# Kernel tuning notes

Hardware: AMD Instinct MI355X
Metric: run time of the kernel (lower is better)

The kernel has to match this reference:

```python
import jax, jax.numpy as jnp
import numpy as np
from jax import lax

NPG = 61      # nodes (electrodes) per graph, hard-coded by 61*hidden reshape
B = 128       # graphs per batch
L = 160       # raw signal length -> final conv length 1
NF = 64       # num_features
HC = 128      # hidden_channels
NCLS = 4


def setup_inputs() -> dict:
    key = jax.random.key(0)
    ks = jax.random.split(key, 16)
    N = B * NPG
    # fully-connected (no self-loops) edges within each graph -> 3660 edges/graph
    a = np.repeat(np.arange(NPG), NPG)
    b = np.tile(np.arange(NPG), NPG)
    m = a != b
    sl, dl = a[m], b[m]
    off = (np.arange(B) * NPG)[:, None]
    edge_index = np.stack([(sl[None] + off).ravel(), (dl[None] + off).ravel()]).astype(np.int64)
    batch = np.repeat(np.arange(B), NPG).astype(np.int64)

    def rn(k, shape, fan_in):
        return jax.random.normal(k, shape, jnp.float32) / np.sqrt(fan_in).astype(np.float32)

    return dict(
        x=jax.random.normal(ks[0], (N, L), jnp.float32),
        edge_index=jnp.asarray(edge_index),
        batch=jnp.asarray(batch),
        edge_features=jax.random.normal(ks[1], (edge_index.shape[1], 3), jnp.float32),
        conv_w0=rn(ks[2], (NF, 1, 7), 7.0), conv_b0=jnp.zeros((NF,), jnp.float32),
        conv_w1=rn(ks[3], (NF, NF, 5), NF * 5.0), conv_b1=jnp.zeros((NF,), jnp.float32),
        conv_w2=rn(ks[4], (NF, NF, 3), NF * 3.0), conv_b2=jnp.zeros((NF,), jnp.float32),
        bn1_g=jnp.ones((NF,), jnp.float32), bn1_b=jnp.zeros((NF,), jnp.float32),
        g_w0=rn(ks[5], (NF, HC), float(NF)), g_b0=jnp.zeros((HC,), jnp.float32),
        g_w1=rn(ks[6], (HC, HC), float(HC)), g_b1=jnp.zeros((HC,), jnp.float32),
        g_w2=rn(ks[7], (HC, HC), float(HC)), g_b2=jnp.zeros((HC,), jnp.float32),
        bn2_g=jnp.ones((HC,), jnp.float32), bn2_b=jnp.zeros((HC,), jnp.float32),
        lin_w0=rn(ks[8], (NPG * HC, HC), float(NPG * HC)), lin_b0=jnp.zeros((HC,), jnp.float32),
        lin_w1=rn(ks[9], (HC, HC), float(HC)), lin_b1=jnp.zeros((HC,), jnp.float32),
        lin_w2=rn(ks[10], (HC, NCLS), float(HC)), lin_b2=jnp.zeros((NCLS,), jnp.float32),
        edge_w=rn(ks[11], (3, 1), 3.0), edge_b=jnp.zeros((1,), jnp.float32),
    )


def _conv1d(x, w, b, pad):
    # x: [N, Cin, L], w: [Cout, Cin, K]
    y = lax.conv_general_dilated(x, w, (1,), [(pad, pad)], dimension_numbers=('NCH', 'OIH', 'NCH'))
    return y + b[None, :, None]


def _maxpool7(x):
    n = x.shape[-1] // 7
    return x[..., : n * 7].reshape(x.shape[0], x.shape[1], n, 7).max(-1)


def _bn(x, g, b):
    # BatchNorm1d in training mode: biased batch statistics
    m = x.mean(0)
    v = x.var(0)
    return (x - m) * lax.rsqrt(v + 1e-5) * g + b


def _forward(x, edge_features, conv_w0, conv_b0, conv_w1, conv_b1, conv_w2, conv_b2,
             bn1_g, bn1_b, g_w0, g_b0, g_w1, g_b1, g_w2, g_b2, bn2_g, bn2_b,
             lin_w0, lin_b0, lin_w1, lin_b1, lin_w2, lin_b2, edge_w, edge_b,
             edge_index, batch):
    N = x.shape[0]
    nb = N // NPG  # == batch.max()+1 for contiguous graph layout
    # tanh-gated edge weights
    ew = jnp.tanh(edge_features @ edge_w + edge_b)            # [E, 1]
    # Conv1d feature extractor: [N,1,160] -> [N,NF,1]
    h = x[:, None, :]
    h = _maxpool7(jax.nn.relu(_conv1d(h, conv_w0, conv_b0, 0)))   # [N,NF,22]
    h = jax.nn.relu(_conv1d(h, conv_w1, conv_b1, 2))               # [N,NF,22]
    h = _maxpool7(h)                                               # [N,NF,3]
    h = _conv1d(h, conv_w2, conv_b2, 0)[:, :, 0]                   # [N,NF]
    h = _bn(h, bn1_g, bn1_b)
    # Edge-weighted GCN hops (MyzConv): lin -> gather src -> scale -> scatter-add dst
    src, dst = edge_index[0], edge_index[1]
    for w, bs, act in ((g_w0, g_b0, True), (g_w1, g_b1, True), (g_w2, g_b2, False)):
        hw = h @ w + bs                                            # [N,HC]
        msg = ew * hw[src]                                         # [E,HC]
        h = jax.ops.segment_sum(msg, dst, num_segments=N)
        if act:
            h = jax.nn.relu(h)
    h = _bn(h, bn2_g, bn2_b)
    # MLP classifier over concatenated node features per graph
    h = h.reshape(nb, NPG * HC)
    h = jax.nn.relu(h @ lin_w0 + lin_b0)
    h = jax.nn.relu(h @ lin_w1 + lin_b1)
    h = h @ lin_w2 + lin_b2
    return jax.nn.log_softmax(h, -1), ew.reshape(nb, -1).T


def reference(x, edge_index, batch, edge_features, conv_w0, conv_b0, conv_w1, conv_b1,
              conv_w2, conv_b2, bn1_g, bn1_b, g_w0, g_b0, g_w1, g_b1, g_w2, g_b2,
              bn2_g, bn2_b, lin_w0, lin_b0, lin_w1, lin_b1, lin_w2, lin_b2, edge_w, edge_b):
    return _forward(x, edge_features, conv_w0, conv_b0, conv_w1, conv_b1, conv_w2, conv_b2,
                    bn1_g, bn1_b, g_w0, g_b0, g_w1, g_b1, g_w2, g_b2, bn2_g, bn2_b,
                    lin_w0, lin_b0, lin_w1, lin_b1, lin_w2, lin_b2, edge_w, edge_b,
                    edge_index, batch)
```

## Files before the change

### kernel.cpp

```cpp
#include <hip/hip_runtime.h>
#include <math.h>

#define NPGN 61
#define NGRAPH 128
#define NNODES (NPGN*NGRAPH)
#define EPG 3660

typedef float float4v __attribute__((ext_vector_type(4)));
typedef short bf16x8 __attribute__((ext_vector_type(8)));
typedef unsigned short u16;

__device__ __forceinline__ u16 f2bf(float v){
  union { float f; unsigned u; } x; x.f = v;
  unsigned r = (x.u + 0x7FFFu + ((x.u >> 16) & 1u)) >> 16;
  return (u16)r;
}
__device__ __forceinline__ float bf2f(unsigned u){
  union { unsigned u; float f; } x; x.u = u << 16;
  return x.f;
}

__global__ __launch_bounds__(256) void k_prep(const float* __restrict__ w0,
    const float* __restrict__ w1, const float* __restrict__ w2,
    const float* __restrict__ gw0, const float* __restrict__ gw1, const float* __restrict__ gw2,
    const float* __restrict__ lw0,
    float* __restrict__ w0t, u16* __restrict__ w1b, u16* __restrict__ w2b,
    u16* __restrict__ gwt0, u16* __restrict__ gwt1, u16* __restrict__ gwt2,
    u16* __restrict__ lw0t){
  __shared__ __align__(16) u16 tile[32*132];
  int b = blockIdx.x, tid = threadIdx.x;
  if (b < 290){
    int idx = b*256 + tid;
    if (idx < 20480){
      int f = idx / 320, r = idx - f*320;
      int kk = r >> 6, c = r & 63;
      w1b[idx] = f2bf(w1[f*320 + c*5 + kk]);
    } else if (idx < 32768){
      int j = idx - 20480; w2b[j] = f2bf(w2[j]);
    } else if (idx < 40960){
      int j = idx - 32768; int jj = j >> 6, k = j & 63; gwt0[j] = f2bf(gw0[k*128 + jj]);
    } else if (idx < 57344){
      int j = idx - 40960; int jj = j >> 7, k = j & 127; gwt1[j] = f2bf(gw1[k*128 + jj]);
    } else if (idx < 73728){
      int j = idx - 57344; int jj = j >> 7, k = j & 127; gwt2[j] = f2bf(gw2[k*128 + jj]);
    } else if (idx < 74176){
      int j = idx - 73728; int k = j >> 6, f = j & 63; w0t[j] = w0[f*7 + k];
    }
  } else {
    int bb = b - 290;
    int i = bb >> 2, oq = bb & 3;
    for (int idx = tid; idx < 4096; idx += 256){
      int k = idx >> 5, ol = idx & 31;
      tile[ol*132 + k] = f2bf(lw0[((size_t)i*128 + k)*128 + oq*32 + ol]);
    }
    __syncthreads();
    unsigned* dst = (unsigned*)lw0t;
    for (int idx = tid; idx < 2048; idx += 256){
      int ol = idx >> 6, kw = idx & 63;
      unsigned v = (unsigned)tile[ol*132 + 2*kw] | ((unsigned)tile[ol*132 + 2*kw + 1] << 16);
      dst[((size_t)i*128 + oq*32 + ol)*64 + kw] = v;
    }
  }
}

#define A0T_STR 72
#define A0T_ROWS 36
#define C1_STR 24
#define NB 4
__global__ __launch_bounds__(256) void k_conv(const float* __restrict__ x,
    const float* __restrict__ w0t, const float* __restrict__ b0,
    const u16* __restrict__ w1b, const float* __restrict__ b1,
    const u16* __restrict__ w2b, const float* __restrict__ b2,
    float* __restrict__ h0, float* __restrict__ stat1p){
  int w = threadIdx.x >> 6, lane = threadIdx.x & 63;
  int tid = threadIdx.x;
  int q = lane >> 4, r16 = lane & 15;
  __shared__ __align__(16) float xs[NB][160];
  __shared__ __align__(16) u16 a0t[A0T_ROWS*A0T_STR];
  __shared__ __align__(16) u16 a1k[208];

  {
    const float* xb = x + (size_t)blockIdx.x*NB*160;
    float* xsf = &xs[0][0];
    #pragma unroll
    for (int idx = tid; idx < NB*160; idx += 256) xsf[idx] = xb[idx];
  }

  bf16x8 wf1[10], wf2[6];
  #pragma unroll
  for (int ks = 0; ks < 10; ks++)
    wf1[ks] = *(const bf16x8*)(w1b + (16*w + r16)*320 + ks*32 + q*8);
  #pragma unroll
  for (int ks = 0; ks < 6; ks++)
    wf2[ks] = *(const bf16x8*)(w2b + (16*w + r16)*192 + ks*32 + q*8);
  float4 b1v = *(const float4*)(b1 + 16*w + 4*q);
  float4 b2v = *(const float4*)(b2 + 16*w + 4*q);

  float w0r[7];
  #pragma unroll
  for (int k = 0; k < 7; k++) w0r[k] = w0t[k*64 + lane];
  float b0f = b0[lane];

  a0t[(24 + w)*A0T_STR + lane] = 0;
  __syncthreads();

  float4v sacc = {0.f,0.f,0.f,0.f}, qacc = {0.f,0.f,0.f,0.f};

  for (int i = 0; i < NB; i++){
    int n = blockIdx.x*NB + i;
    const float* xsp = &xs[i][0];

    if (w < 2) a0t[w*A0T_STR + lane] = 0;

    for (int qp = w; qp < 11; qp += 4){
      float win[20];
      #pragma unroll
      for (int j = 0; j < 20; j++) win[j] = xsp[14*qp + j];
      float m0, m1;
      #pragma unroll
      for (int r = 0; r < 7; r++){
        float s = w0r[0]*win[r];
        #pragma unroll
        for (int k = 1; k < 7; k++) s += w0r[k]*win[r+k];
        m0 = r ? fmaxf(m0, s) : s;
      }
      #pragma unroll
      for (int r = 7; r < 14; r++){
        float s = w0r[0]*win[r];
        #pragma unroll
        for (int k = 1; k < 7; k++) s += w0r[k]*win[r+k];
        m1 = (r > 7) ? fmaxf(m1, s) : s;
      }
      a0t[(2 + 2*qp)*A0T_STR + lane] = f2bf(fmaxf(m0 + b0f, 0.f));
      a0t[(3 + 2*qp)*A0T_STR + lane] = f2bf(fmaxf(m1 + b0f, 0.f));
    }
    __syncthreads();

    float4v acc0 = {0.f,0.f,0.f,0.f}, acc1 = {0.f,0.f,0.f,0.f};
    #pragma unroll
    for (int ks = 0; ks < 10; ks++){
      int kk = ks >> 1;
      int cbase = (ks & 1)*32 + q*8;
      bf16x8 bv0 = *(const bf16x8*)(a0t + (r16 + kk)*A0T_STR + cbase);
      bf16x8 bv1 = *(const bf16x8*)(a0t + (r16 + 16 + kk)*A0T_STR + cbase);
      acc0 = __builtin_amdgcn_mfma_f32_16x16x32_bf16(wf1[ks], bv0, acc0, 0, 0, 0);
      acc1 = __builtin_amdgcn_mfma_f32_16x16x32_bf16(wf1[ks], bv1, acc1, 0, 0, 0);
    }
    __syncthreads();

    u16* c1 = a0t;
    #pragma unroll
    for (int reg = 0; reg < 4; reg++){
      int m = 16*w + q*4 + reg;
      float bv_ = ((const float*)&b1v)[reg];
      c1[m*C1_STR + r16] = f2bf(fmaxf(acc0[reg] + bv_, 0.f));
      if (r16 <= 4)
        c1[m*C1_STR + 16 + r16] = f2bf(fmaxf(acc1[reg] + bv_, 0.f));
    }
    __syncthreads();

    if (w == (i & 3)){
      bf16x8 f0 = *(const bf16x8*)(c1 + lane*C1_STR);
      bf16x8 f1 = *(const bf16x8*)(c1 + lane*C1_STR + 8);
      bf16x8 f2 = *(const bf16x8*)(c1 + lane*C1_STR + 16);
      float v[24];
      #pragma unroll
      for (int j = 0; j < 8; j++){
        v[j]    = bf2f((u16)f0[j]);
        v[8+j]  = bf2f((u16)f1[j]);
        v[16+j] = bf2f((u16)f2[j]);
      }
      #pragma unroll
      for (int t = 0; t < 3; t++){
        float m = v[t*7];
        #pragma unroll
        for (int r = 1; r < 7; r++) m = fmaxf(m, v[t*7+r]);
        a1k[lane*3 + t] = f2bf(m);
      }
    }
    __syncthreads();

    float4v acc2 = {0.f,0.f,0.f,0.f};
    #pragma unroll
    for (int ks = 0; ks < 6; ks++){
      bf16x8 bs = *(const bf16x8*)(a1k + ks*32 + q*8);
      acc2 = __builtin_amdgcn_mfma_f32_16x16x32_bf16(wf2[ks], bs, acc2, 0, 0, 0);
    }
    if (r16 == 0){
      #pragma unroll
      for (int reg = 0; reg < 4; reg++){
        int f = 16*w + 4*q + reg;
        float v = acc2[reg] + ((const float*)&b2v)[reg];
        h0[(size_t)n*64 + f] = v;
        sacc[reg] += v;
        qacc[reg] += v*v;
      }
    }
  }

  if (r16 == 0){
    int bkt = blockIdx.x & 31;
    #pragma unroll
    for (int reg = 0; reg < 4; reg++){
      int f = 16*w + 4*q + reg;
      atomicAdd(&stat1p[bkt*128 + f], sacc[reg]);
      atomicAdd(&stat1p[bkt*128 + 64 + f], qacc[reg]);
    }
  }
}

#define EW_STR 72
#define HS_STR 136
#define HWT_STR 72
__global__ __launch_bounds__(512) void k_gnn(const float* __restrict__ h0,
    const float* __restrict__ stat1p,
    const float* __restrict__ bn1g, const float* __restrict__ bn1b,
    const u16* __restrict__ gwt0, const float* __restrict__ gb0,
    const u16* __restrict__ gwt1, const float* __restrict__ gb1,
    const u16* __restrict__ gwt2, const float* __restrict__ gb2,
    const float* __restrict__ ef, const float* __restrict__ eww,
    const float* __restrict__ ewb, float* __restrict__ out2,
    u16* __restrict__ hB, float* __restrict__ stat2p){
  int g = blockIdx.x, tid = threadIdx.x;
  int w = tid >> 6, lane = tid & 63, q = lane >> 4, r16 = lane & 15;
  int dt = w & 3, jh = w >> 2;
  __shared__ u16 hs[64*HS_STR];
  __shared__ u16 hwT[128*HWT_STR];
  __shared__ u16 ewl[64*EW_STR];
  __shared__ float bsc[64], bsh[64];
  __shared__ float st2[256];

  bf16x8 af0[2], af1[4], af2[4];
  #pragma unroll
  for (int ks = 0; ks < 2; ks++)
    af0[ks] = *(const bf16x8*)(gwt0 + (16*w + r16)*64 + ks*32 + q*8);
  #pragma unroll
  for (int ks = 0; ks < 4; ks++)
    af1[ks] = *(const bf16x8*)(gwt1 + (16*w + r16)*128 + ks*32 + q*8);
  #pragma unroll
  for (int ks = 0; ks < 4; ks++)
    af2[ks] = *(const bf16x8*)(gwt2 + (16*w + r16)*128 + ks*32 + q*8);
  float4 b40 = *(const float4*)(gb0 + 16*w + 4*q);
  float4 b41 = *(const float4*)(gb1 + 16*w + 4*q);
  float4 b42 = *(const float4*)(gb2 + 16*w + 4*q);

  if (tid < 64){
    float s = 0.f, s2 = 0.f;
    #pragma unroll
    for (int r = 0; r < 32; r++){
      s  += stat1p[r*128 + tid];
      s2 += stat1p[r*128 + 64 + tid];
    }
    float m = s*(1.f/NNODES), v = s2*(1.f/NNODES) - m*m;
    float sc = rsqrtf(v + 1e-5f)*bn1g[tid];
    bsc[tid] = sc; bsh[tid] = bn1b[tid] - m*sc;
  }
  if (tid < 256) st2[tid] = 0.f;
  {
    unsigned* td = (unsigned*)ewl;
    for (int idx = tid; idx < 64*EW_STR/2; idx += 512) td[idx] = 0;
  }
  {
    unsigned* hsd = (unsigned*)hs;
    for (int idx = tid; idx < 3*(HS_STR/2); idx += 512){
      int rr = 61 + idx/(HS_STR/2), cc = idx%(HS_STR/2);
      hsd[rr*(HS_STR/2) + cc] = 0;
    }
  }
  __syncthreads();

  {
    float v0 = eww[0], v1 = eww[1], v2 = eww[2], bb = ewb[0];
    const float* efg = ef + (size_t)g*EPG*3;
    for (int idx = tid; idx < EPG; idx += 512){
      const float* p = efg + idx*3;
      float v = tanhf(p[0]*v0 + p[1]*v1 + p[2]*v2 + bb);
      int s = idx/60, r = idx - s*60;
      int d = r + (r >= s ? 1 : 0);
      ewl[d*EW_STR + s] = f2bf(v);
      out2[(size_t)idx*128 + g] = v;
    }
  }
  {
    unsigned* hsd = (unsigned*)hs;
    for (int idx = tid; idx < 61*32; idx += 512){
      int i = idx >> 5, kw = idx & 31;
      float2 hv = *(const float2*)(h0 + ((size_t)g*61 + i)*64 + kw*2);
      int k0 = kw*2;
      float a = hv.x*bsc[k0] + bsh[k0];
      float b = hv.y*bsc[k0+1] + bsh[k0+1];
      hsd[i*(HS_STR/2) + kw] = (unsigned)f2bf(a) | ((unsigned)f2bf(b) << 16);
    }
  }
  __syncthreads();
  bf16x8 ewf[2];
  #pragma unroll
  for (int ks = 0; ks < 2; ks++)
    ewf[ks] = *(const bf16x8*)(ewl + (16*dt + r16)*EW_STR + ks*32 + q*8);

  #pragma unroll
  for (int nt = 0; nt < 4; nt++){
    float4v acc = {b40.x, b40.y, b40.z, b40.w};
    #pragma unroll
    for (int ks = 0; ks < 2; ks++){
      bf16x8 bv = *(const bf16x8*)(hs + (nt*16 + r16)*HS_STR + ks*32 + q*8);
      acc = __builtin_amdgcn_mfma_f32_16x16x32_bf16(af0[ks], bv, acc, 0, 0, 0);
    }
    #pragma unroll
    for (int r = 0; r < 4; r++)
      hwT[(16*w + 4*q + r)*HWT_STR + nt*16 + r16] = f2bf(acc[r]);
  }
  __syncthreads();
  #pragma unroll
  for (int nt = 0; nt < 4; nt++){
    int j = (jh*4 + nt)*16;
    float4v acc = {0.f,0.f,0.f,0.f};
    #pragma unroll
    for (int ks = 0; ks < 2; ks++){
      bf16x8 bv = *(const bf16x8*)(hwT + (j + r16)*HWT_STR + ks*32 + q*8);
      acc = __builtin_amdgcn_mfma_f32_16x16x32_bf16(ewf[ks], bv, acc, 0, 0, 0);
    }
    #pragma unroll
    for (int r = 0; r < 4; r++){
      int d = 16*dt + 4*q + r;
      hs[d*HS_STR + j + r16] = f2bf(fmaxf(acc[r], 0.f));
    }
  }
  __syncthreads();

  #pragma unroll
  for (int nt = 0; nt < 4; nt++){
    float4v acc = {b41.x, b41.y, b41.z, b41.w};
    #pragma unroll
    for (int ks = 0; ks < 4; ks++){
      bf16x8 bv = *(const bf16x8*)(hs + (nt*16 + r16)*HS_STR + ks*32 + q*8);
      acc = __builtin_amdgcn_mfma_f32_16x16x32_bf16(af1[ks], bv, acc, 0, 0, 0);
    }
    #pragma unroll
    for (int r = 0; r < 4; r++)
      hwT[(16*w + 4*q + r)*HWT_STR + nt*16 + r16] = f2bf(acc[r]);
  }
  __syncthreads();
  #pragma unroll
  for (int nt = 0; nt < 4; nt++){
    int j = (jh*4 + nt)*16;
    float4v acc = {0.f,0.f,0.f,0.f};
    #pragma unroll
    for (int ks = 0; ks < 2; ks++){
      bf16x8 bv = *(const bf16x8*)(hwT + (j + r16)*HWT_STR + ks*32 + q*8);
      acc = __builtin_amdgcn_mfma_f32_16x16x32_bf16(ewf[ks], bv, acc, 0, 0, 0);
    }
    #pragma unroll
    for (int r = 0; r < 4; r++){
      int d = 16*dt + 4*q + r;
      hs[d*HS_STR + j + r16] = f2bf(fmaxf(acc[r], 0.f));
    }
  }
  __syncthreads();

  #pragma unroll
  for (int nt = 0; nt < 4; nt++){
    float4v acc = {b42.x, b42.y, b42.z, b42.w};
    #pragma unroll
    for (int ks = 0; ks < 4; ks++){
      bf16x8 bv = *(const bf16x8*)(hs + (nt*16 + r16)*HS_STR + ks*32 + q*8);
      acc = __builtin_amdgcn_mfma_f32_16x16x32_bf16(af2[ks], bv, acc, 0, 0, 0);
    }
    #pragma unroll
    for (int r = 0; r < 4; r++)
      hwT[(16*w + 4*q + r)*HWT_STR + nt*16 + r16] = f2bf(acc[r]);
  }
  __syncthreads();
  #pragma unroll
  for (int nt = 0; nt < 4; nt++){
    int j = (jh*4 + nt)*16;
    float4v acc = {0.f,0.f,0.f,0.f};
    #pragma unroll
    for (int ks = 0; ks < 2; ks++){
      bf16x8 bv = *(const bf16x8*)(hwT + (j + r16)*HWT_STR + ks*32 + q*8);
      acc = __builtin_amdgcn_mfma_f32_16x16x32_bf16(ewf[ks], bv, acc, 0, 0, 0);
    }
    float cs = 0.f, cq = 0.f;
    #pragma unroll
    for (int r = 0; r < 4; r++){
      int d = 16*dt + 4*q + r;
      if (d < 61){
        float v = acc[r];
        hB[((size_t)g*61 + d)*128 + j + r16] = f2bf(v);
        cs += v; cq += v*v;
      }
    }
    int col = j + r16;
    atomicAdd(&st2[col], cs);
    atomicAdd(&st2[128 + col], cq);
  }
  __syncthreads();
  if (tid < 256) stat2p[(size_t)tid*128 + g] = st2[tid];
}

#define AS_STR 136
__global__ __launch_bounds__(256) void k_mlp0(const u16* __restrict__ hB,
    const float* __restrict__ stat2p,
    const float* __restrict__ bn2g, const float* __restrict__ bn2b,
    const u16* __restrict__ lw0t, float* __restrict__ y0pre){
  int bi = blockIdx.x; int i = bi >> 2, sub = bi & 3;
  int oh = sub & 1, gh = sub >> 1;
  int tid = threadIdx.x, w = tid >> 6, lane = tid & 63, q = lane >> 4, r16 = lane & 15;
  __shared__ u16 As[64*AS_STR];
  __shared__ float sc2[128], sh2[128];
  if (tid < 128){
    float4v sa = {0,0,0,0}, sb = {0,0,0,0};
    #pragma unroll
    for (int r = 0; r < 32; r++){
      sa += *(const float4v*)(stat2p + (size_t)tid*128 + r*4);
      sb += *(const float4v*)(stat2p + (size_t)(128 + tid)*128 + r*4);
    }
    float s = sa[0]+sa[1]+sa[2]+sa[3], s2 = sb[0]+sb[1]+sb[2]+sb[3];
    float m = s*(1.f/NNODES), v = s2*(1.f/NNODES) - m*m;
    float sc = rsqrtf(v + 1e-5f)*bn2g[tid];
    sc2[tid] = sc; sh2[tid] = bn2b[tid] - m*sc;
  }
  __syncthreads();
  {
    const unsigned* hbd = (const unsigned*)hB;
    unsigned* asd = (unsigned*)As;
    for (int idx = tid; idx < 4096; idx += 256){
      int gg = gh*64 + (idx >> 6), kw = idx & 63;
      unsigned pv = hbd[((size_t)gg*61 + i)*64 + kw];
      int k0 = kw*2;
      float a = bf2f(pv & 0xffffu)*sc2[k0] + sh2[k0];
      float b = bf2f(pv >> 16)*sc2[k0+1] + sh2[k0+1];
      asd[(idx >> 6)*(AS_STR/2) + kw] = (unsigned)f2bf(a) | ((unsigned)f2bf(b) << 16);
    }
  }
  __syncthreads();
  const u16* wbase = lw0t + ((size_t)i*128 + oh*64)*128;
  bf16x8 af[4];
  #pragma unroll
  for (int ks = 0; ks < 4; ks++)
    af[ks] = *(const bf16x8*)(As + (16*w + r16)*AS_STR + ks*32 + q*8);
  #pragma unroll
  for (int nt = 0; nt < 4; nt++){
    float4v acc = {0.f,0.f,0.f,0.f};
    #pragma unroll
    for (int ks = 0; ks < 4; ks++){
      bf16x8 bv = *(const bf16x8*)(wbase + (size_t)(nt*16 + r16)*128 + ks*32 + q*8);
      acc = __builtin_amdgcn_mfma_f32_16x16x32_bf16(af[ks], bv, acc, 0, 0, 0);
    }
    #pragma unroll
    for (int r = 0; r < 4; r++){
      int g = gh*64 + 16*w + 4*q + r;
      atomicAdd(&y0pre[(size_t)g*128 + oh*64 + nt*16 + r16], acc[r]);
    }
  }
}

__global__ __launch_bounds__(128) void k_mlp1(const float* __restrict__ y0pre,
    const float* __restrict__ lb0, const float* __restrict__ W1,
    const float* __restrict__ lb1, const float* __restrict__ W2,
    const float* __restrict__ lb2, float* __restrict__ out){
  int g = blockIdx.x, o = threadIdx.x;
  __shared__ float y0[128], y1[128], red[128];
  y0[o] = fmaxf(y0pre[(size_t)g*128 + o] + lb0[o], 0.f);
  __syncthreads();
  float a = lb1[o];
  #pragma unroll 8
  for (int k = 0; k < 128; k++) a += y0[k]*W1[k*128 + o];
  y1[o] = fmaxf(a, 0.f);
  __syncthreads();
  int c = o & 3, kb = o >> 2;
  float a2 = 0.f;
  #pragma unroll
  for (int j = 0; j < 4; j++){
    int k = kb + 32*j;
    a2 += y1[k]*W2[k*4 + c];
  }
  red[o] = a2;
  __syncthreads();
  #pragma unroll
  for (int off = 64; off >= 4; off >>= 1){
    if (o < off) red[o] += red[o + off];
    __syncthreads();
  }
  if (o == 0){
    float v0 = red[0]+lb2[0], v1 = red[1]+lb2[1], v2 = red[2]+lb2[2], v3 = red[3]+lb2[3];
    float m = fmaxf(fmaxf(v0,v1), fmaxf(v2,v3));
    float lse = m + logf(expf(v0-m)+expf(v1-m)+expf(v2-m)+expf(v3-m));
    out[g*4+0]=v0-lse; out[g*4+1]=v1-lse; out[g*4+2]=v2-lse; out[g*4+3]=v3-lse;
  }
}

extern "C" void kernel_launch(void* const* d_in, const int* in_sizes, int n_in,
                              void* d_out, int out_size, void* d_ws, size_t ws_size,
                              hipStream_t stream){
  const float* x    = (const float*)d_in[0];
  const float* ef   = (const float*)d_in[3];
  const float* cw0  = (const float*)d_in[4];
  const float* cb0  = (const float*)d_in[5];
  const float* cw1  = (const float*)d_in[6];
  const float* cb1  = (const float*)d_in[7];
  const float* cw2  = (const float*)d_in[8];
  const float* cb2  = (const float*)d_in[9];
  const float* bn1g = (const float*)d_in[10];
  const float* bn1b = (const float*)d_in[11];
  const float* gw0  = (const float*)d_in[12];
  const float* gb0  = (const float*)d_in[13];
  const float* gw1  = (const float*)d_in[14];
  const float* gb1  = (const float*)d_in[15];
  const float* gw2  = (const float*)d_in[16];
  const float* gb2  = (const float*)d_in[17];
  const float* bn2g = (const float*)d_in[18];
  const float* bn2b = (const float*)d_in[19];
  const float* lw0  = (const float*)d_in[20];
  const float* lb0  = (const float*)d_in[21];
  const float* lw1  = (const float*)d_in[22];
  const float* lb1  = (const float*)d_in[23];
  const float* lw2  = (const float*)d_in[24];
  const float* lb2  = (const float*)d_in[25];
  const float* eww  = (const float*)d_in[26];
  const float* ewb  = (const float*)d_in[27];
  float* out = (float*)d_out;

  float* ws   = (float*)d_ws;
  float* w1s  = ws;
  float* w2s  = w1s + 10240;
  float* w0t  = w2s + 6144;
  float* gws0 = w0t + 448;
  float* gws1 = gws0 + 4096;
  float* gws2 = gws1 + 8192;
  float* h0   = gws2 + 8192;
  float* hBs  = h0 + 499712;
  float* lw0s = hBs + 499712;
  float* accs = lw0s + 499712;

  u16* w1b    = (u16*)w1s;
  u16* w2b    = (u16*)w2s;
  u16* gwt0   = (u16*)gws0;
  u16* gwt1   = (u16*)gws1;
  u16* gwt2   = (u16*)gws2;
  u16* hB     = (u16*)hBs;
  u16* lw0t   = (u16*)lw0s;
  float* stat1p = accs;
  float* y0pre  = accs + 4096;
  float* stat2p = accs + 20480;

  hipMemsetAsync(accs, 0, 20480*sizeof(float), stream);
  k_prep <<<534, 256, 0, stream>>>(cw0, cw1, cw2, gw0, gw1, gw2, lw0,
                                   w0t, w1b, w2b, gwt0, gwt1, gwt2, lw0t);
  k_conv <<<NNODES/NB, 256, 0, stream>>>(x, w0t, cb0, w1b, cb1, w2b, cb2, h0, stat1p);
  k_gnn  <<<NGRAPH, 512, 0, stream>>>(h0, stat1p, bn1g, bn1b,
                                      gwt0, gb0, gwt1, gb1, gwt2, gb2,
                                      ef, eww, ewb, out + 512, hB, stat2p);
  k_mlp0 <<<NPGN*4, 256, 0, stream>>>(hB, stat2p, bn2g, bn2b, lw0t, y0pre);
  k_mlp1 <<<NGRAPH, 128, 0, stream>>>(y0pre, lb0, lw1, lb1, lw2, lb2, out);
}
```

Baseline: 202.2 us.

## Batch conv stages across all nodes per block to cut barriers

```diff
diff --git a/kernel.cpp b/kernel.cpp
--- a/kernel.cpp
+++ b/kernel.cpp
@@ -64,7 +64,6 @@
 }
 
 #define A0T_STR 72
-#define A0T_ROWS 36
 #define C1_STR 24
 #define NB 4
 __global__ __launch_bounds__(256) void k_conv(const float* __restrict__ x,
@@ -76,8 +75,9 @@
   int tid = threadIdx.x;
   int q = lane >> 4, r16 = lane & 15;
   __shared__ __align__(16) float xs[NB][160];
-  __shared__ __align__(16) u16 a0t[A0T_ROWS*A0T_STR];
-  __shared__ __align__(16) u16 a1k[208];
+  __shared__ __align__(16) u16 a0t[NB][36*A0T_STR];
+  __shared__ __align__(16) u16 c1s[NB][64*C1_STR];
+  __shared__ __align__(16) u16 a1k[NB][208];
 
   {
     const float* xb = x + (size_t)blockIdx.x*NB*160;
@@ -101,97 +101,100 @@
   for (int k = 0; k < 7; k++) w0r[k] = w0t[k*64 + lane];
   float b0f = b0[lane];
 
-  a0t[(24 + w)*A0T_STR + lane] = 0;
-  __syncthreads();
-
-  float4v sacc = {0.f,0.f,0.f,0.f}, qacc = {0.f,0.f,0.f,0.f};
-
-  for (int i = 0; i < NB; i++){
-    int n = blockIdx.x*NB + i;
-    const float* xsp = &xs[i][0];
-
-    if (w < 2) a0t[w*A0T_STR + lane] = 0;
-
-    for (int qp = w; qp < 11; qp += 4){
-      float win[20];
+  #pragma unroll
+  for (int i2 = 0; i2 < 6; i2++){
+    int rp = (i2 < 2) ? i2 : 22 + i2;
+    a0t[w][rp*A0T_STR + lane] = 0;
+  }
+  __syncthreads();
+
+  for (int j = w; j < 44; j += 4){
+    int n = j / 11, qp = j - n*11;
+    const float* xsp = &xs[n][0];
+    float win[20];
+    #pragma unroll
+    for (int jj = 0; jj < 20; jj++) win[jj] = xsp[14*qp + jj];
+    float m0, m1;
+    #pragma unroll
+    for (int r = 0; r < 7; r++){
+      float s = w0r[0]*win[r];
       #pragma unroll
-      for (int j = 0; j < 20; j++) win[j] = xsp[14*qp + j];
-      float m0, m1;
+      for (int k = 1; k < 7; k++) s += w0r[k]*win[r+k];
+      m0 = r ? fmaxf(m0, s) : s;
+    }
+    #pragma unroll
+    for (int r = 7; r < 14; r++){
+      float s = w0r[0]*win[r];
       #pragma unroll
-      for (int r = 0; r < 7; r++){
-        float s = w0r[0]*win[r];
-        #pragma unroll
-        for (int k = 1; k < 7; k++) s += w0r[k]*win[r+k];
-        m0 = r ? fmaxf(m0, s) : s;
-      }
-      #pragma unroll
-      for (int r = 7; r < 14; r++){
-        float s = w0r[0]*win[r];
-        #pragma unroll
-        for (int k = 1; k < 7; k++) s += w0r[k]*win[r+k];
-        m1 = (r > 7) ? fmaxf(m1, s) : s;
-      }
-      a0t[(2 + 2*qp)*A0T_STR + lane] = f2bf(fmaxf(m0 + b0f, 0.f));
-      a0t[(3 + 2*qp)*A0T_STR + lane] = f2bf(fmaxf(m1 + b0f, 0.f));
-    }
-    __syncthreads();
-
+      for (int k = 1; k < 7; k++) s += w0r[k]*win[r+k];
+      m1 = (r > 7) ? fmaxf(m1, s) : s;
+    }
+    a0t[n][(2 + 2*qp)*A0T_STR + lane] = f2bf(fmaxf(m0 + b0f, 0.f));
+    a0t[n][(3 + 2*qp)*A0T_STR + lane] = f2bf(fmaxf(m1 + b0f, 0.f));
+  }
+  __syncthreads();
+
+  #pragma unroll 1
+  for (int n = 0; n < NB; n++){
     float4v acc0 = {0.f,0.f,0.f,0.f}, acc1 = {0.f,0.f,0.f,0.f};
     #pragma unroll
     for (int ks = 0; ks < 10; ks++){
       int kk = ks >> 1;
       int cbase = (ks & 1)*32 + q*8;
-      bf16x8 bv0 = *(const bf16x8*)(a0t + (r16 + kk)*A0T_STR + cbase);
-      bf16x8 bv1 = *(const bf16x8*)(a0t + (r16 + 16 + kk)*A0T_STR + cbase);
+      bf16x8 bv0 = *(const bf16x8*)(&a0t[n][(r16 + kk)*A0T_STR + cbase]);
+      bf16x8 bv1 = *(const bf16x8*)(&a0t[n][(r16 + 16 + kk)*A0T_STR + cbase]);
       acc0 = __builtin_amdgcn_mfma_f32_16x16x32_bf16(wf1[ks], bv0, acc0, 0, 0, 0);
       acc1 = __builtin_amdgcn_mfma_f32_16x16x32_bf16(wf1[ks], bv1, acc1, 0, 0, 0);
     }
-    __syncthreads();
-
-    u16* c1 = a0t;
     #pragma unroll
     for (int reg = 0; reg < 4; reg++){
       int m = 16*w + q*4 + reg;
       float bv_ = ((const float*)&b1v)[reg];
-      c1[m*C1_STR + r16] = f2bf(fmaxf(acc0[reg] + bv_, 0.f));
+      c1s[n][m*C1_STR + r16] = f2bf(fmaxf(acc0[reg] + bv_, 0.f));
       if (r16 <= 4)
-        c1[m*C1_STR + 16 + r16] = f2bf(fmaxf(acc1[reg] + bv_, 0.f));
-    }
-    __syncthreads();
-
-    if (w == (i & 3)){
-      bf16x8 f0 = *(const bf16x8*)(c1 + lane*C1_STR);
-      bf16x8 f1 = *(const bf16x8*)(c1 + lane*C1_STR + 8);
-      bf16x8 f2 = *(const bf16x8*)(c1 + lane*C1_STR + 16);
-      float v[24];
+        c1s[n][m*C1_STR + 16 + r16] = f2bf(fmaxf(acc1[reg] + bv_, 0.f));
+    }
+  }
+  __syncthreads();
+
+  {
+    const u16* c1 = &c1s[w][0];
+    bf16x8 f0 = *(const bf16x8*)(c1 + lane*C1_STR);
+    bf16x8 f1 = *(const bf16x8*)(c1 + lane*C1_STR + 8);
+    bf16x8 f2 = *(const bf16x8*)(c1 + lane*C1_STR + 16);
+    float v[24];
+    #pragma unroll
+    for (int j = 0; j < 8; j++){
+      v[j]    = bf2f((u16)f0[j]);
+      v[8+j]  = bf2f((u16)f1[j]);
+      v[16+j] = bf2f((u16)f2[j]);
+    }
+    #pragma unroll
+    for (int t = 0; t < 3; t++){
+      float m = v[t*7];
       #pragma unroll
-      for (int j = 0; j < 8; j++){
-        v[j]    = bf2f((u16)f0[j]);
-        v[8+j]  = bf2f((u16)f1[j]);
-        v[16+j] = bf2f((u16)f2[j]);
-      }
-      #pragma unroll
-      for (int t = 0; t < 3; t++){
-        float m = v[t*7];
-        #pragma unroll
-        for (int r = 1; r < 7; r++) m = fmaxf(m, v[t*7+r]);
-        a1k[lane*3 + t] = f2bf(m);
-      }
-    }
-    __syncthreads();
-
+      for (int r = 1; r < 7; r++) m = fmaxf(m, v[t*7+r]);
+      a1k[w][lane*3 + t] = f2bf(m);
+    }
+  }
+  __syncthreads();
+
+  float4v sacc = {0.f,0.f,0.f,0.f}, qacc = {0.f,0.f,0.f,0.f};
+  #pragma unroll 1
+  for (int n = 0; n < NB; n++){
     float4v acc2 = {0.f,0.f,0.f,0.f};
     #pragma unroll
     for (int ks = 0; ks < 6; ks++){
-      bf16x8 bs = *(const bf16x8*)(a1k + ks*32 + q*8);
+      bf16x8 bs = *(const bf16x8*)(&a1k[n][ks*32 + q*8]);
       acc2 = __builtin_amdgcn_mfma_f32_16x16x32_bf16(wf2[ks], bs, acc2, 0, 0, 0);
     }
     if (r16 == 0){
+      int nn = blockIdx.x*NB + n;
       #pragma unroll
       for (int reg = 0; reg < 4; reg++){
         int f = 16*w + 4*q + reg;
         float v = acc2[reg] + ((const float*)&b2v)[reg];
-        h0[(size_t)n*64 + f] = v;
+        h0[(size_t)nn*64 + f] = v;
         sacc[reg] += v;
         qacc[reg] += v*v;
       }
```

After: 199.1 us. Within noise of the previous version (-1.5%).
